# Kernel optimization log

Hardware: AMD Instinct MI355X
Metric: run time of the kernel (lower is better)

Reference implementation:

```python
import jax, jax.numpy as jnp
import numpy as np

V = 6890            # FAUST mesh vertices (also n_classes of the dense head)
C_IN = 3            # raw xyz signal
R, A = 5, 8         # kernel_size = (n_radial, n_angular)
ROT_DELTA = 1
ROTS = tuple(range(0, A, ROT_DELTA))  # 8 rotations
DIMS = [100, 100, 100]
EPS_BN = 1e-3       # keras BatchNormalization default epsilon


def setup_inputs() -> dict:
    key = jax.random.key(0)
    ks = jax.random.split(key, 12)
    inp = {}
    inp["signal"] = jax.random.normal(ks[0], (V, C_IN), jnp.float32)
    inp["bc_idx"] = jax.random.randint(ks[1], (V, R, A, 3), 0, V, dtype=jnp.int32)
    w = jax.random.uniform(ks[2], (V, R, A, 3), jnp.float32)
    inp["bc_w"] = w / jnp.sum(w, axis=-1, keepdims=True)  # convex barycentric weights
    # keras Normalization (not adapted): mean=0, var=1
    inp["norm_mean"] = jnp.zeros((C_IN,), jnp.float32)
    inp["norm_var"] = jnp.ones((C_IN,), jnp.float32)
    # ConvDirac templates: (amt_templates, n_radial, n_angular, c_in) + bias
    cins = [C_IN] + DIMS[:-1]
    for i, (ci, t) in enumerate(zip(cins, DIMS)):
        inp[f"w{i}"] = jax.random.normal(ks[3 + i], (t, R, A, ci), jnp.float32) * 0.05
        inp[f"b{i}"] = jnp.zeros((t,), jnp.float32)
    # BatchNorm (inference mode) params, stacked over the 3 blocks
    inp["bn_gamma"] = jnp.ones((3, DIMS[0]), jnp.float32)
    inp["bn_beta"] = jnp.zeros((3, DIMS[0]), jnp.float32)
    inp["bn_mean"] = jax.random.normal(ks[6], (3, DIMS[0]), jnp.float32) * 0.01
    inp["bn_var"] = jnp.ones((3, DIMS[0]), jnp.float32)
    inp["dense_w"] = jax.random.normal(ks[7], (DIMS[-1], V), jnp.float32) * 0.02
    inp["dense_b"] = jnp.zeros((V,), jnp.float32)
    return inp


def _isc_dirac(sig, bc_idx, bc_w, W, b):
    """Intrinsic surface conv (Dirac): barycentric patch gather + multi-rotation fold.
    sig: (V, C); bc_idx/bc_w: (V, R, A, 3); W: (T, R, A, C); b: (T,)
    returns (V, n_rot, T) after relu."""
    # patch operator: interpolate signal at template vertices -> (V, R, A, C)
    patch = jnp.einsum('vraic,vrai->vrac', sig[bc_idx], bc_w)
    # rotate the (small) template over the angular axis instead of the patch
    Wrot = jnp.stack([jnp.roll(W, -r, axis=2) for r in ROTS])  # (n_rot, T, R, A, C)
    out = jnp.einsum('vrac,ntrac->vnt', patch, Wrot) + b
    return jax.nn.relu(out)


def _amp(x):
    """AngularMaxPooling: keep the rotation response with max L2 norm. x: (V, n_rot, T)."""
    idx = jnp.argmax(jnp.linalg.norm(x, axis=-1), axis=-1)  # (V,)
    return jnp.take_along_axis(x, idx[:, None, None], axis=1)[:, 0, :]


def _bn(x, g, b, m, v):
    return g * (x - m) * jax.lax.rsqrt(v + EPS_BN) + b


def reference(signal, bc_idx, bc_w, norm_mean, norm_var, w0, b0, w1, b1, w2, b2,
              bn_gamma, bn_beta, bn_mean, bn_var, dense_w, dense_b):
    x = (signal - norm_mean) / jnp.sqrt(norm_var)
    for i, (W, b) in enumerate(((w0, b0), (w1, b1), (w2, b2))):
        x = _isc_dirac(x, bc_idx, bc_w, W, b)      # (V, n_rot, T)
        x = _amp(x)                                 # (V, T)
        x = _bn(x, bn_gamma[i], bn_beta[i], bn_mean[i], bn_var[i])
        # dropout: identity at inference
    return x @ dense_w + dense_b                    # (V, 6890)
```

## Files before the change

kernel.cpp:

```cpp
#include <hip/hip_runtime.h>

#define VN 6890
#define TN 100
#define NOUT 800
#define MP 6912
#define NP 896
#define CONVSZ (MP * NP)

typedef __attribute__((ext_vector_type(8))) short bf16x8;
typedef __attribute__((ext_vector_type(4))) float f32x4;

__device__ __forceinline__ unsigned short f2bf(float f) {
    unsigned u = __float_as_uint(f);
    return (unsigned short)((u + 0x7FFFu + ((u >> 16) & 1u)) >> 16);
}
__device__ __forceinline__ void split_bf16(float f, short* h, short* l) {
    unsigned short hb = f2bf(f);
    float hf = __uint_as_float(((unsigned)hb) << 16);
    *h = (short)hb;
    *l = (short)f2bf(f - hf);
}
__device__ __forceinline__ void gload16(const short* g, void* lds) {
    __builtin_amdgcn_global_load_lds(
        (const __attribute__((address_space(1))) void*)g,
        (__attribute__((address_space(3))) void*)lds, 16, 0, 0);
}

__global__ __launch_bounds__(256) void norm_kernel(
    const float* __restrict__ sig, const float* __restrict__ mean,
    const float* __restrict__ var, float* __restrict__ x0)
{
    int i = blockIdx.x * blockDim.x + threadIdx.x;
    if (i < VN * 3) {
        int c = i % 3;
        x0[i] = (sig[i] - mean[c]) / sqrtf(var[c]);
    }
}

template<int CIN, int KPAD>
__global__ __launch_bounds__(256) void rotw_split(
    const float* __restrict__ W, short* __restrict__ Bh, short* __restrict__ Bl)
{
    const int n = blockIdx.x;
    const int K = 40 * CIN;
    const int rot = n / TN, t = n - rot * TN;
    for (int k = threadIdx.x; k < KPAD; k += 256) {
        float w = 0.f;
        if (n < NOUT && k < K) {
            int ra = k / CIN, c = k - ra * CIN;
            int r = ra >> 3, a = ra & 7;
            int a2 = (a + rot) & 7;
            w = W[((t * 5 + r) * 8 + a2) * CIN + c];
        }
        short h, l; split_bf16(w, &h, &l);
        Bh[(size_t)n * KPAD + k] = h;
        Bl[(size_t)n * KPAD + k] = l;
    }
}

template<int CIN, int KPAD>
__global__ __launch_bounds__(256) void patch_split(
    const float* __restrict__ x, const int* __restrict__ bidx,
    const float* __restrict__ bw, short* __restrict__ Ph, short* __restrict__ Pl)
{
    __shared__ int   sIdx[120];
    __shared__ float sW[120];
    const int v = blockIdx.x;
    const int tid = threadIdx.x;
    const int K = 40 * CIN;
    if (v >= VN) {
        for (int e = tid; e < KPAD; e += 256) {
            Ph[(size_t)v * KPAD + e] = 0;
            Pl[(size_t)v * KPAD + e] = 0;
        }
        return;
    }
    if (tid < 120) { sIdx[tid] = bidx[v * 120 + tid]; sW[tid] = bw[v * 120 + tid]; }
    __syncthreads();
    for (int e = tid; e < KPAD; e += 256) {
        float s = 0.f;
        if (e < K) {
            int ra = e / CIN, c = e - ra * CIN;
            s = sW[ra * 3 + 0] * x[sIdx[ra * 3 + 0] * CIN + c]
              + sW[ra * 3 + 1] * x[sIdx[ra * 3 + 1] * CIN + c]
              + sW[ra * 3 + 2] * x[sIdx[ra * 3 + 2] * CIN + c];
        }
        short h, l; split_bf16(s, &h, &l);
        Ph[(size_t)v * KPAD + e] = h;
        Pl[(size_t)v * KPAD + e] = l;
    }
}

template<bool CONV_EPI>
__global__ __launch_bounds__(256, 2) void mfma_gemm(
    const short* __restrict__ Ah, const short* __restrict__ Al,
    const short* __restrict__ Bh, const short* __restrict__ Bl,
    const float* __restrict__ bias, float* __restrict__ C,
    int M, int N, int ldc, int K, int Ksl, int cstride)
{
    __shared__ __align__(16) short AhS[4096];
    __shared__ __align__(16) short AlS[4096];
    __shared__ __align__(16) short BhS[4096];
    __shared__ __align__(16) short BlS[4096];

    const int tid  = threadIdx.x;
    const int wave = tid >> 6;
    const int lane = tid & 63;
    const int lr = lane & 15, lg = lane >> 4;
    const int wm = wave >> 1, wn = wave & 1;
    const int m0 = blockIdx.x * 128;
    const int n0 = blockIdx.y * 128;
    const int kbase = blockIdx.z * Ksl;
    const int kcnt  = min(Ksl, K - kbase);
    if (CONV_EPI) C += (size_t)blockIdx.z * cstride;

    const int off0 = tid * 16, off1 = off0 + 4096;
    const int row0 = off0 >> 6, row1 = off1 >> 6;
    const int g0 = ((off0 >> 4) & 3) ^ ((row0 >> 1) & 3);
    const int g1 = ((off1 >> 4) & 3) ^ ((row1 >> 1) & 3);
    const size_t aO0 = (size_t)(m0 + row0) * K + kbase + g0 * 8;
    const size_t aO1 = (size_t)(m0 + row1) * K + kbase + g1 * 8;
    const size_t bO0 = (size_t)(n0 + row0) * K + kbase + g0 * 8;
    const size_t bO1 = (size_t)(n0 + row1) * K + kbase + g1 * 8;
    const int wofs = wave << 10;

    int aRd[4], bRd[4];
    #pragma unroll
    for (int f = 0; f < 4; ++f) {
        int ar = wm * 64 + f * 16 + lr;
        aRd[f] = ar * 64 + ((lg ^ ((ar >> 1) & 3)) << 4);
        int br = wn * 64 + f * 16 + lr;
        bRd[f] = br * 64 + ((lg ^ ((br >> 1) & 3)) << 4);
    }

    f32x4 acc[4][4];
    #pragma unroll
    for (int i = 0; i < 4; ++i)
        #pragma unroll
        for (int j = 0; j < 4; ++j)
            acc[i][j] = (f32x4){0.f, 0.f, 0.f, 0.f};

    const int nkt = kcnt >> 5;
    for (int kt = 0; kt < nkt; ++kt) {
        const int k0 = kt << 5;
        gload16(Ah + aO0 + k0, (char*)AhS + wofs);
        gload16(Ah + aO1 + k0, (char*)AhS + 4096 + wofs);
        gload16(Al + aO0 + k0, (char*)AlS + wofs);
        gload16(Al + aO1 + k0, (char*)AlS + 4096 + wofs);
        gload16(Bh + bO0 + k0, (char*)BhS + wofs);
        gload16(Bh + bO1 + k0, (char*)BhS + 4096 + wofs);
        gload16(Bl + bO0 + k0, (char*)BlS + wofs);
        gload16(Bl + bO1 + k0, (char*)BlS + 4096 + wofs);
        __syncthreads();

        bf16x8 ah[4], al[4], bh[4], bl[4];
        #pragma unroll
        for (int f = 0; f < 4; ++f) {
            ah[f] = *(const bf16x8*)((const char*)AhS + aRd[f]);
            al[f] = *(const bf16x8*)((const char*)AlS + aRd[f]);
            bh[f] = *(const bf16x8*)((const char*)BhS + bRd[f]);
            bl[f] = *(const bf16x8*)((const char*)BlS + bRd[f]);
        }
        #pragma unroll
        for (int i = 0; i < 4; ++i)
            #pragma unroll
            for (int j = 0; j < 4; ++j)
                acc[i][j] = __builtin_amdgcn_mfma_f32_16x16x32_bf16(ah[i], bh[j], acc[i][j], 0, 0, 0);
        #pragma unroll
        for (int i = 0; i < 4; ++i)
            #pragma unroll
            for (int j = 0; j < 4; ++j)
                acc[i][j] = __builtin_amdgcn_mfma_f32_16x16x32_bf16(ah[i], bl[j], acc[i][j], 0, 0, 0);
        #pragma unroll
        for (int i = 0; i < 4; ++i)
            #pragma unroll
            for (int j = 0; j < 4; ++j)
                acc[i][j] = __builtin_amdgcn_mfma_f32_16x16x32_bf16(al[i], bh[j], acc[i][j], 0, 0, 0);
        __syncthreads();
    }

    #pragma unroll
    for (int i = 0; i < 4; ++i) {
        const int mb = m0 + wm * 64 + i * 16 + lg * 4;
        #pragma unroll
        for (int j = 0; j < 4; ++j) {
            const int n = n0 + wn * 64 + j * 16 + lr;
            if (CONV_EPI) {
                #pragma unroll
                for (int q = 0; q < 4; ++q)
                    C[(size_t)(mb + q) * ldc + n] = acc[i][j][q];
            } else {
                if (n < N) {
                    const float bv = bias[n];
                    #pragma unroll
                    for (int q = 0; q < 4; ++q)
                        if (mb + q < M)
                            C[(size_t)(mb + q) * ldc + n] = acc[i][j][q] + bv;
                }
            }
        }
    }
}

template<bool CONV_EPI>
__global__ __launch_bounds__(256, 4) void tile_gemm(
    const float* __restrict__ A, const float* __restrict__ B,
    const float* __restrict__ bias, float* __restrict__ C,
    int M, int N, int K)
{
    __shared__ __align__(16) float As[32][132];
    __shared__ __align__(16) float Bs[32][68];

    const int tid = threadIdx.x;
    const int m0 = blockIdx.x * 128;
    const int n0 = blockIdx.y * 64;
    const int ty = tid >> 4;
    const int tx = tid & 15;
    const int nkt = (K + 31) >> 5;

    float4 aR[4];
    float2 bR[4];

    auto load_tile = [&](int kt) {
        const int k0 = kt << 5;
        #pragma unroll
        for (int j = 0; j < 4; ++j) {
            int q = tid + 256 * j;
            int row = q >> 3, kq = (q & 7) << 2;
            int v = m0 + row, k = k0 + kq;
            if (v < M && k < K)
                aR[j] = *reinterpret_cast<const float4*>(A + (size_t)v * K + k);
            else
                aR[j] = make_float4(0.f, 0.f, 0.f, 0.f);
        }
        #pragma unroll
        for (int j = 0; j < 2; ++j) {
            int q = tid + 256 * j;
            int krow = q >> 4, nq = (q & 15) << 2;
            int k = k0 + krow, n = n0 + nq;
            bR[2 * j]     = (k < K && n + 1 < N)
                ? *reinterpret_cast<const float2*>(B + (size_t)k * N + n)     : make_float2(0.f, 0.f);
            bR[2 * j + 1] = (k < K && n + 3 < N)
                ? *reinterpret_cast<const float2*>(B + (size_t)k * N + n + 2) : make_float2(0.f, 0.f);
        }
    };
    auto stage = [&]() {
        #pragma unroll
        for (int j = 0; j < 4; ++j) {
            int q = tid + 256 * j;
            int row = q >> 3, kq = (q & 7) << 2;
            As[kq + 0][row] = aR[j].x; As[kq + 1][row] = aR[j].y;
            As[kq + 2][row] = aR[j].z; As[kq + 3][row] = aR[j].w;
        }
        #pragma unroll
        for (int j = 0; j < 2; ++j) {
            int q = tid + 256 * j;
            int krow = q >> 4, nq = (q & 15) << 2;
            *reinterpret_cast<float2*>(&Bs[krow][nq])     = bR[2 * j];
            *reinterpret_cast<float2*>(&Bs[krow][nq + 2]) = bR[2 * j + 1];
        }
    };

    float acc[8][4];
    #pragma unroll
    for (int i = 0; i < 8; ++i)
        #pragma unroll
        for (int j = 0; j < 4; ++j) acc[i][j] = 0.f;

    load_tile(0);
    stage();
    __syncthreads();

    for (int kt = 0; kt < nkt; ++kt) {
        if (kt + 1 < nkt) load_tile(kt + 1);
        #pragma unroll 16
        for (int k = 0; k < 32; ++k) {
            float4 a0 = *reinterpret_cast<const float4*>(&As[k][ty * 8]);
            float4 a1 = *reinterpret_cast<const float4*>(&As[k][ty * 8 + 4]);
            float4 b  = *reinterpret_cast<const float4*>(&Bs[k][tx * 4]);
            float av[8] = {a0.x, a0.y, a0.z, a0.w, a1.x, a1.y, a1.z, a1.w};
            float bv[4] = {b.x, b.y, b.z, b.w};
            #pragma unroll
            for (int i = 0; i < 8; ++i)
                #pragma unroll
                for (int j = 0; j < 4; ++j)
                    acc[i][j] = fmaf(av[i], bv[j], acc[i][j]);
        }
        __syncthreads();
        if (kt + 1 < nkt) { stage(); __syncthreads(); }
    }

    #pragma unroll
    for (int i = 0; i < 8; ++i) {
        int vr = m0 + ty * 8 + i;
        if (vr >= M) continue;
        int nb = n0 + tx * 4;
        size_t base = (size_t)vr * N + nb;
        if (nb + 1 < N) {
            float2 o = {acc[i][0] + bias[nb], acc[i][1] + bias[nb + 1]};
            *reinterpret_cast<float2*>(C + base) = o;
        }
        if (nb + 3 < N) {
            float2 o = {acc[i][2] + bias[nb + 2], acc[i][3] + bias[nb + 3]};
            *reinterpret_cast<float2*>(C + base + 2) = o;
        }
    }
}

__global__ __launch_bounds__(256) void amp_bn(
    const float* __restrict__ conv,
    const float* __restrict__ bias,
    const float* __restrict__ g,  const float* __restrict__ be,
    const float* __restrict__ mu, const float* __restrict__ var,
    float* __restrict__ xout)
{
    int v = blockIdx.x * 4 + (threadIdx.x >> 6);
    int lane = threadIdx.x & 63;
    if (v >= VN) return;
    const float* y0 = conv + (size_t)v * NP;
    const float* y1 = y0 + CONVSZ;

    const float bLo = bias[lane];
    const float bHi = (lane < 36) ? bias[64 + lane] : 0.f;

    float t1[8], t2[8], s[8];
    #pragma unroll
    for (int n = 0; n < 8; ++n) {
        float a = fmaxf(y0[n * TN + lane] + y1[n * TN + lane] + bLo, 0.f);
        float b = (lane < 36)
            ? fmaxf(y0[n * TN + 64 + lane] + y1[n * TN + 64 + lane] + bHi, 0.f) : 0.f;
        t1[n] = a; t2[n] = b;
        s[n] = a * a + b * b;
    }
    #pragma unroll
    for (int off = 32; off > 0; off >>= 1)
        #pragma unroll
        for (int n = 0; n < 8; ++n) s[n] += __shfl_xor(s[n], off);

    int best = 0; float bs = s[0];
    #pragma unroll
    for (int n = 1; n < 8; ++n) { if (s[n] > bs) { bs = s[n]; best = n; } }

    float a = t1[0], b = t2[0];
    #pragma unroll
    for (int n = 1; n < 8; ++n) { if (best == n) { a = t1[n]; b = t2[n]; } }

    {
        float inv = 1.0f / sqrtf(var[lane] + 1e-3f);
        xout[v * TN + lane] = g[lane] * (a - mu[lane]) * inv + be[lane];
    }
    if (lane < 36) {
        int t = 64 + lane;
        float inv = 1.0f / sqrtf(var[t] + 1e-3f);
        xout[v * TN + t] = g[t] * (b - mu[t]) * inv + be[t];
    }
}

__global__ __launch_bounds__(256) void dense_a_split(
    const float* __restrict__ xA, short* __restrict__ Ah, short* __restrict__ Al)
{
    int i = blockIdx.x * 256 + threadIdx.x;
    if (i >= MP * 128) return;
    int v = i >> 7, k = i & 127;
    float f = (v < VN && k < TN) ? xA[v * TN + k] : 0.f;
    short h, l; split_bf16(f, &h, &l);
    Ah[i] = h; Al[i] = l;
}
__global__ __launch_bounds__(256) void dense_b_split(
    const float* __restrict__ dw, short* __restrict__ Bh, short* __restrict__ Bl)
{
    int i = blockIdx.x * 256 + threadIdx.x;
    if (i >= MP * 128) return;
    int n = i >> 7, k = i & 127;
    float f = (n < VN && k < TN) ? dw[(size_t)k * VN + n] : 0.f;
    short h, l; split_bf16(f, &h, &l);
    Bh[i] = h; Bl[i] = l;
}

extern "C" void kernel_launch(void* const* d_in, const int* in_sizes, int n_in,
                              void* d_out, int out_size, void* d_ws, size_t ws_size,
                              hipStream_t stream) {
    const float* signal = (const float*)d_in[0];
    const int*   bcix   = (const int*)  d_in[1];
    const float* bcw    = (const float*)d_in[2];
    const float* nmean  = (const float*)d_in[3];
    const float* nvar   = (const float*)d_in[4];
    const float* w0     = (const float*)d_in[5];
    const float* b0     = (const float*)d_in[6];
    const float* w1     = (const float*)d_in[7];
    const float* b1     = (const float*)d_in[8];
    const float* w2     = (const float*)d_in[9];
    const float* b2     = (const float*)d_in[10];
    const float* bng    = (const float*)d_in[11];
    const float* bnb    = (const float*)d_in[12];
    const float* bnm    = (const float*)d_in[13];
    const float* bnv    = (const float*)d_in[14];
    const float* dw     = (const float*)d_in[15];
    const float* db     = (const float*)d_in[16];
    float* out = (float*)d_out;

    float* x0 = (float*)d_ws;
    float* xA = x0 + 20736;
    float* xB = xA + 689024;
    short* dAh = (short*)xB;
    short* dAl = dAh + (size_t)MP * 128;
    short* dBh = dAl + (size_t)MP * 128;
    short* dBl = dBh + (size_t)MP * 128;
    const size_t ws_need = (size_t)709760 * 4 + (size_t)4 * MP * 128 * 2;
    const bool dense_mfma = ws_size >= ws_need;

    short* Ph  = (short*)out;
    short* Pl  = Ph  + (size_t)MP * 4000;
    short* Bth = Pl  + (size_t)MP * 4000;
    short* Btl = Bth + (size_t)NP * 4000;
    float* conv = out + (size_t)MP * 4000 + (size_t)NP * 4000;

    dim3 cgrid(MP / 128, NP / 128, 2);
    dim3 mgrid(MP / 128, MP / 128, 1);
    dim3 dgrid((VN + 127) / 128, (VN + 63) / 64);
    int ampg = (VN + 3) / 4;

    norm_kernel<<<(VN * 3 + 255) / 256, 256, 0, stream>>>(signal, nmean, nvar, x0);

    rotw_split<3, 128><<<NP, 256, 0, stream>>>(w0, Bth, Btl);
    patch_split<3, 128><<<MP, 256, 0, stream>>>(x0, bcix, bcw, Ph, Pl);
    mfma_gemm<true><<<cgrid, 256, 0, stream>>>(Ph, Pl, Bth, Btl, b0, conv, VN, NOUT, NP, 128, 64, CONVSZ);
    amp_bn<<<ampg, 256, 0, stream>>>(conv, b0, bng, bnb, bnm, bnv, xA);

    rotw_split<100, 4000><<<NP, 256, 0, stream>>>(w1, Bth, Btl);
    patch_split<100, 4000><<<MP, 256, 0, stream>>>(xA, bcix, bcw, Ph, Pl);
    mfma_gemm<true><<<cgrid, 256, 0, stream>>>(Ph, Pl, Bth, Btl, b1, conv, VN, NOUT, NP, 4000, 2016, CONVSZ);
    amp_bn<<<ampg, 256, 0, stream>>>(conv, b1, bng + 100, bnb + 100, bnm + 100, bnv + 100, xB);

    rotw_split<100, 4000><<<NP, 256, 0, stream>>>(w2, Bth, Btl);
    patch_split<100, 4000><<<MP, 256, 0, stream>>>(xB, bcix, bcw, Ph, Pl);
    mfma_gemm<true><<<cgrid, 256, 0, stream>>>(Ph, Pl, Bth, Btl, b2, conv, VN, NOUT, NP, 4000, 2016, CONVSZ);
    amp_bn<<<ampg, 256, 0, stream>>>(conv, b2, bng + 200, bnb + 200, bnm + 200, bnv + 200, xA);

    if (dense_mfma) {
        dense_a_split<<<(MP * 128 + 255) / 256, 256, 0, stream>>>(xA, dAh, dAl);
        dense_b_split<<<(MP * 128 + 255) / 256, 256, 0, stream>>>(dw, dBh, dBl);
        mfma_gemm<false><<<mgrid, 256, 0, stream>>>(dAh, dAl, dBh, dBl, db, out, VN, VN, VN, 128, 128, 0);
    } else {
        tile_gemm<false><<<dgrid, 256, 0, stream>>>(xA, dw, db, out, VN, VN, TN);
    }
}
```

Before: 756.3 us.

## Add 512-thread triple-buffered split-bf16 MFMA GEMM for hidden conv layers

Adds a new conv GEMM kernel that runs 8 waves per 128x128 tile. It uses a three-stage LDS ring filled by direct global-to-LDS loads, staggers the hi/lo operand loads between the three MFMA phases, and raises wave priority around the MFMA bursts. Layers 1 and 2 switch to this kernel, with the same split-K of 2. The aim is to hide global-load latency behind MFMA work in the dominant K=4000 GEMMs. In exchange it uses 96KB of LDS per block, runs one block per CU, and adds more barriers per k-step.

```diff
diff --git a/kernel.cpp b/kernel.cpp
--- a/kernel.cpp
+++ b/kernel.cpp
@@ -9,6 +9,8 @@
 
 typedef __attribute__((ext_vector_type(8))) short bf16x8;
 typedef __attribute__((ext_vector_type(4))) float f32x4;
+
+#define BAR() do { asm volatile("" ::: "memory"); __builtin_amdgcn_s_barrier(); asm volatile("" ::: "memory"); } while (0)
 
 __device__ __forceinline__ unsigned short f2bf(float f) {
     unsigned u = __float_as_uint(f);
@@ -202,6 +204,189 @@
     }
 }
 
+__global__ __launch_bounds__(512, 1) void mfma_conv512(
+    const short* __restrict__ Ah, const short* __restrict__ Al,
+    const short* __restrict__ Bh, const short* __restrict__ Bl,
+    float* __restrict__ C, int K, int Ksl, int cstride)
+{
+    __shared__ __align__(16) short LDS[3 * 4 * 4096];
+
+    const int tid = threadIdx.x;
+    const int w = tid >> 6, lane = tid & 63;
+    const int lr = lane & 15, lg = lane >> 4;
+    const int wm = w >> 2, wn = w & 3;
+    const int m0 = blockIdx.x * 128;
+    const int n0 = blockIdx.y * 128;
+    const int kbase = blockIdx.z * Ksl;
+    const int kcnt = min(Ksl, K - kbase);
+    C += (size_t)blockIdx.z * cstride;
+
+    const int srow = tid >> 2;
+    const int sg   = (tid & 3) ^ ((srow >> 1) & 3);
+    const size_t aO = (size_t)(m0 + srow) * K + kbase + sg * 8;
+    const size_t bO = (size_t)(n0 + srow) * K + kbase + sg * 8;
+    const int wdst = w << 9;
+
+    int aRd[4], bRd[2];
+    #pragma unroll
+    for (int i = 0; i < 4; ++i) {
+        int ar = wm * 64 + i * 16 + lr;
+        aRd[i] = ar * 64 + ((lg ^ ((ar >> 1) & 3)) << 4);
+    }
+    #pragma unroll
+    for (int j = 0; j < 2; ++j) {
+        int br = wn * 32 + j * 16 + lr;
+        bRd[j] = br * 64 + ((lg ^ ((br >> 1) & 3)) << 4);
+    }
+
+    f32x4 acc[4][2];
+    #pragma unroll
+    for (int i = 0; i < 4; ++i)
+        #pragma unroll
+        for (int j = 0; j < 2; ++j)
+            acc[i][j] = (f32x4){0.f, 0.f, 0.f, 0.f};
+
+    const int nt = kcnt >> 5;
+
+    auto REG = [&](int b, int r) -> short* { return &LDS[(b * 4 + r) * 4096]; };
+
+    {
+        gload16(Ah + aO,      REG(0, 0) + wdst);
+        gload16(Al + aO,      REG(0, 1) + wdst);
+        gload16(Bh + bO,      REG(0, 2) + wdst);
+        gload16(Bl + bO,      REG(0, 3) + wdst);
+        if (nt > 1) {
+            gload16(Ah + aO + 32, REG(1, 0) + wdst);
+            gload16(Al + aO + 32, REG(1, 1) + wdst);
+            gload16(Bh + bO + 32, REG(1, 2) + wdst);
+            gload16(Bl + bO + 32, REG(1, 3) + wdst);
+        }
+    }
+
+    int cur = 0;
+    for (int t = 0; t < nt; ++t) {
+        const char* LAh = (const char*)REG(cur, 0);
+        const char* LAl = (const char*)REG(cur, 1);
+        const char* LBh = (const char*)REG(cur, 2);
+        const char* LBl = (const char*)REG(cur, 3);
+        const int nb = (t + 2) % 3;
+        const int kn = (t + 2) << 5;
+
+        if (t + 2 < nt) {
+            gload16(Ah + aO + kn, REG(nb, 0) + wdst);
+            gload16(Bh + bO + kn, REG(nb, 2) + wdst);
+            asm volatile("s_waitcnt vmcnt(6)" ::: "memory");
+        } else if (t + 1 < nt) {
+            asm volatile("s_waitcnt vmcnt(4)" ::: "memory");
+        } else {
+            asm volatile("s_waitcnt vmcnt(0)" ::: "memory");
+        }
+        BAR();
+        bf16x8 ah[4], bh[2], bl[2], al[4];
+        #pragma unroll
+        for (int i = 0; i < 4; ++i) ah[i] = *(const bf16x8*)(LAh + aRd[i]);
+        #pragma unroll
+        for (int j = 0; j < 2; ++j) bh[j] = *(const bf16x8*)(LBh + bRd[j]);
+        __builtin_amdgcn_s_setprio(1);
+        #pragma unroll
+        for (int i = 0; i < 4; ++i)
+            #pragma unroll
+            for (int j = 0; j < 2; ++j)
+                acc[i][j] = __builtin_amdgcn_mfma_f32_16x16x32_bf16(ah[i], bh[j], acc[i][j], 0, 0, 0);
+        __builtin_amdgcn_s_setprio(0);
+        BAR();
+
+        #pragma unroll
+        for (int j = 0; j < 2; ++j) bl[j] = *(const bf16x8*)(LBl + bRd[j]);
+        if (t + 2 < nt) gload16(Al + aO + kn, REG(nb, 1) + wdst);
+        BAR();
+        __builtin_amdgcn_s_setprio(1);
+        #pragma unroll
+        for (int i = 0; i < 4; ++i)
+            #pragma unroll
+            for (int j = 0; j < 2; ++j)
+                acc[i][j] = __builtin_amdgcn_mfma_f32_16x16x32_bf16(ah[i], bl[j], acc[i][j], 0, 0, 0);
+        __builtin_amdgcn_s_setprio(0);
+        BAR();
+
+        #pragma unroll
+        for (int i = 0; i < 4; ++i) al[i] = *(const bf16x8*)(LAl + aRd[i]);
+        if (t + 2 < nt) gload16(Bl + bO + kn, REG(nb, 3) + wdst);
+        BAR();
+        __builtin_amdgcn_s_setprio(1);
+        #pragma unroll
+        for (int i = 0; i < 4; ++i)
+            #pragma unroll
+            for (int j = 0; j < 2; ++j)
+                acc[i][j] = __builtin_amdgcn_mfma_f32_16x16x32_bf16(al[i], bh[j], acc[i][j], 0, 0, 0);
+        __builtin_amdgcn_s_setprio(0);
+        BAR();
+
+        cur = (cur + 1 == 3) ? 0 : cur + 1;
+    }
+
+    #pragma unroll
+    for (int i = 0; i < 4; ++i) {
+        const int mb = m0 + wm * 64 + i * 16 + lg * 4;
+        #pragma unroll
+        for (int j = 0; j < 2; ++j) {
+            const int n = n0 + wn * 32 + j * 16 + lr;
+            #pragma unroll
+            for (int q = 0; q < 4; ++q)
+                C[(size_t)(mb + q) * NP + n] = acc[i][j][q];
+        }
+    }
+}
+
+__global__ __launch_bounds__(256) void amp_bn(
+    const float* __restrict__ conv,
+    const float* __restrict__ bias,
+    const float* __restrict__ g,  const float* __restrict__ be,
+    const float* __restrict__ mu, const float* __restrict__ var,
+    float* __restrict__ xout)
+{
+    int v = blockIdx.x * 4 + (threadIdx.x >> 6);
+    int lane = threadIdx.x & 63;
+    if (v >= VN) return;
+    const float* y0 = conv + (size_t)v * NP;
+    const float* y1 = y0 + CONVSZ;
+
+    const float bLo = bias[lane];
+    const float bHi = (lane < 36) ? bias[64 + lane] : 0.f;
+
+    float t1[8], t2[8], s[8];
+    #pragma unroll
+    for (int n = 0; n < 8; ++n) {
+        float a = fmaxf(y0[n * TN + lane] + y1[n * TN + lane] + bLo, 0.f);
+        float b = (lane < 36)
+            ? fmaxf(y0[n * TN + 64 + lane] + y1[n * TN + 64 + lane] + bHi, 0.f) : 0.f;
+        t1[n] = a; t2[n] = b;
+        s[n] = a * a + b * b;
+    }
+    #pragma unroll
+    for (int off = 32; off > 0; off >>= 1)
+        #pragma unroll
+        for (int n = 0; n < 8; ++n) s[n] += __shfl_xor(s[n], off);
+
+    int best = 0; float bs = s[0];
+    #pragma unroll
+    for (int n = 1; n < 8; ++n) { if (s[n] > bs) { bs = s[n]; best = n; } }
+
+    float a = t1[0], b = t2[0];
+    #pragma unroll
+    for (int n = 1; n < 8; ++n) { if (best == n) { a = t1[n]; b = t2[n]; } }
+
+    {
+        float inv = 1.0f / sqrtf(var[lane] + 1e-3f);
+        xout[v * TN + lane] = g[lane] * (a - mu[lane]) * inv + be[lane];
+    }
+    if (lane < 36) {
+        int t = 64 + lane;
+        float inv = 1.0f / sqrtf(var[t] + 1e-3f);
+        xout[v * TN + t] = g[t] * (b - mu[t]) * inv + be[t];
+    }
+}
+
 template<bool CONV_EPI>
 __global__ __launch_bounds__(256, 4) void tile_gemm(
     const float* __restrict__ A, const float* __restrict__ B,
@@ -304,55 +489,6 @@
             float2 o = {acc[i][2] + bias[nb + 2], acc[i][3] + bias[nb + 3]};
             *reinterpret_cast<float2*>(C + base + 2) = o;
         }
-    }
-}
-
-__global__ __launch_bounds__(256) void amp_bn(
-    const float* __restrict__ conv,
-    const float* __restrict__ bias,
-    const float* __restrict__ g,  const float* __restrict__ be,
-    const float* __restrict__ mu, const float* __restrict__ var,
-    float* __restrict__ xout)
-{
-    int v = blockIdx.x * 4 + (threadIdx.x >> 6);
-    int lane = threadIdx.x & 63;
-    if (v >= VN) return;
-    const float* y0 = conv + (size_t)v * NP;
-    const float* y1 = y0 + CONVSZ;
-
-    const float bLo = bias[lane];
-    const float bHi = (lane < 36) ? bias[64 + lane] : 0.f;
-
-    float t1[8], t2[8], s[8];
-    #pragma unroll
-    for (int n = 0; n < 8; ++n) {
-        float a = fmaxf(y0[n * TN + lane] + y1[n * TN + lane] + bLo, 0.f);
-        float b = (lane < 36)
-            ? fmaxf(y0[n * TN + 64 + lane] + y1[n * TN + 64 + lane] + bHi, 0.f) : 0.f;
-        t1[n] = a; t2[n] = b;
-        s[n] = a * a + b * b;
-    }
-    #pragma unroll
-    for (int off = 32; off > 0; off >>= 1)
-        #pragma unroll
-        for (int n = 0; n < 8; ++n) s[n] += __shfl_xor(s[n], off);
-
-    int best = 0; float bs = s[0];
-    #pragma unroll
-    for (int n = 1; n < 8; ++n) { if (s[n] > bs) { bs = s[n]; best = n; } }
-
-    float a = t1[0], b = t2[0];
-    #pragma unroll
-    for (int n = 1; n < 8; ++n) { if (best == n) { a = t1[n]; b = t2[n]; } }
-
-    {
-        float inv = 1.0f / sqrtf(var[lane] + 1e-3f);
-        xout[v * TN + lane] = g[lane] * (a - mu[lane]) * inv + be[lane];
-    }
-    if (lane < 36) {
-        int t = 64 + lane;
-        float inv = 1.0f / sqrtf(var[t] + 1e-3f);
-        xout[v * TN + t] = g[t] * (b - mu[t]) * inv + be[t];
     }
 }
 
@@ -416,6 +552,7 @@
     float* conv = out + (size_t)MP * 4000 + (size_t)NP * 4000;
 
     dim3 cgrid(MP / 128, NP / 128, 2);
+    dim3 c8grid(MP / 128, NP / 128, 2);
     dim3 mgrid(MP / 128, MP / 128, 1);
     dim3 dgrid((VN + 127) / 128, (VN + 63) / 64);
     int ampg = (VN + 3) / 4;
@@ -429,12 +566,12 @@
 
     rotw_split<100, 4000><<<NP, 256, 0, stream>>>(w1, Bth, Btl);
     patch_split<100, 4000><<<MP, 256, 0, stream>>>(xA, bcix, bcw, Ph, Pl);
-    mfma_gemm<true><<<cgrid, 256, 0, stream>>>(Ph, Pl, Bth, Btl, b1, conv, VN, NOUT, NP, 4000, 2016, CONVSZ);
+    mfma_conv512<<<c8grid, 512, 0, stream>>>(Ph, Pl, Bth, Btl, conv, 4000, 2016, CONVSZ);
     amp_bn<<<ampg, 256, 0, stream>>>(conv, b1, bng + 100, bnb + 100, bnm + 100, bnv + 100, xB);
 
     rotw_split<100, 4000><<<NP, 256, 0, stream>>>(w2, Bth, Btl);
     patch_split<100, 4000><<<MP, 256, 0, stream>>>(xB, bcix, bcw, Ph, Pl);
-    mfma_gemm<true><<<cgrid, 256, 0, stream>>>(Ph, Pl, Bth, Btl, b2, conv, VN, NOUT, NP, 4000, 2016, CONVSZ);
+    mfma_conv512<<<c8grid, 512, 0, stream>>>(Ph, Pl, Bth, Btl, conv, 4000, 2016, CONVSZ);
     amp_bn<<<ampg, 256, 0, stream>>>(conv, b2, bng + 200, bnb + 200, bnm + 200, bnv + 200, xA);
 
     if (dense_mfma) {
```

After: 742.3 us. Within noise of the previous version (-1.9%).

## Add triple-buffered split-bf16 MFMA GEMM for the 100-channel conv layers

Applied to the files above, without the earlier changes.

Adds a new conv_tri kernel for layers 1 and 2. It uses a three-stage LDS ring filled by direct global-to-LDS loads, with explicit vmcnt waits and a single barrier per K step, so the next two tiles load while MFMAs run. The launch grid is transposed (N-tiles on x, M-tiles on y), which changes block scheduling and cache reuse of the patch matrix. The trade-off is 96KB of LDS per block, which limits occupancy to one block per CU, plus a reliance on hand-placed waitcnt correctness.

```diff
diff --git a/kernel.cpp b/kernel.cpp
--- a/kernel.cpp
+++ b/kernel.cpp
@@ -9,6 +9,8 @@
 
 typedef __attribute__((ext_vector_type(8))) short bf16x8;
 typedef __attribute__((ext_vector_type(4))) float f32x4;
+
+#define BAR() do { asm volatile("" ::: "memory"); __builtin_amdgcn_s_barrier(); asm volatile("" ::: "memory"); } while (0)
 
 __device__ __forceinline__ unsigned short f2bf(float f) {
     unsigned u = __float_as_uint(f);
@@ -202,6 +204,163 @@
     }
 }
 
+__global__ __launch_bounds__(256, 1) void conv_tri(
+    const short* __restrict__ Ah, const short* __restrict__ Al,
+    const short* __restrict__ Bh, const short* __restrict__ Bl,
+    float* __restrict__ C, int K, int Ksl, int cstride)
+{
+    __shared__ __align__(16) short LDS[3 * 4 * 4096];
+
+    const int tid  = threadIdx.x;
+    const int wave = tid >> 6;
+    const int lane = tid & 63;
+    const int lr = lane & 15, lg = lane >> 4;
+    const int wm = wave >> 1, wn = wave & 1;
+    const int n0 = blockIdx.x * 128;
+    const int m0 = blockIdx.y * 128;
+    const int kbase = blockIdx.z * Ksl;
+    const int kcnt  = min(Ksl, K - kbase);
+    C += (size_t)blockIdx.z * cstride;
+
+    const int off0 = tid * 16, off1 = off0 + 4096;
+    const int row0 = off0 >> 6, row1 = off1 >> 6;
+    const int g0 = ((off0 >> 4) & 3) ^ ((row0 >> 1) & 3);
+    const int g1 = ((off1 >> 4) & 3) ^ ((row1 >> 1) & 3);
+    const size_t aO0 = (size_t)(m0 + row0) * K + kbase + g0 * 8;
+    const size_t aO1 = (size_t)(m0 + row1) * K + kbase + g1 * 8;
+    const size_t bO0 = (size_t)(n0 + row0) * K + kbase + g0 * 8;
+    const size_t bO1 = (size_t)(n0 + row1) * K + kbase + g1 * 8;
+    const int wofs = wave << 10;
+
+    int aRd[4], bRd[4];
+    #pragma unroll
+    for (int f = 0; f < 4; ++f) {
+        int ar = wm * 64 + f * 16 + lr;
+        aRd[f] = ar * 64 + ((lg ^ ((ar >> 1) & 3)) << 4);
+        int br = wn * 64 + f * 16 + lr;
+        bRd[f] = br * 64 + ((lg ^ ((br >> 1) & 3)) << 4);
+    }
+
+    f32x4 acc[4][4];
+    #pragma unroll
+    for (int i = 0; i < 4; ++i)
+        #pragma unroll
+        for (int j = 0; j < 4; ++j)
+            acc[i][j] = (f32x4){0.f, 0.f, 0.f, 0.f};
+
+    const int nt = kcnt >> 5;
+
+    auto issue = [&](int x) {
+        char* buf = (char*)LDS + (x % 3) * 32768;
+        const int k0 = x << 5;
+        gload16(Ah + aO0 + k0, buf + wofs);
+        gload16(Ah + aO1 + k0, buf + 4096 + wofs);
+        gload16(Al + aO0 + k0, buf + 8192 + wofs);
+        gload16(Al + aO1 + k0, buf + 8192 + 4096 + wofs);
+        gload16(Bh + bO0 + k0, buf + 16384 + wofs);
+        gload16(Bh + bO1 + k0, buf + 16384 + 4096 + wofs);
+        gload16(Bl + bO0 + k0, buf + 24576 + wofs);
+        gload16(Bl + bO1 + k0, buf + 24576 + 4096 + wofs);
+    };
+
+    issue(0);
+    if (nt > 1) issue(1);
+
+    for (int t = 0; t < nt; ++t) {
+        if (t + 1 < nt) { asm volatile("s_waitcnt vmcnt(8)" ::: "memory"); }
+        else            { asm volatile("s_waitcnt vmcnt(0)" ::: "memory"); }
+        BAR();
+
+        const char* buf = (const char*)LDS + (t % 3) * 32768;
+        bf16x8 ah[4], al[4], bh[4], bl[4];
+        #pragma unroll
+        for (int f = 0; f < 4; ++f) {
+            ah[f] = *(const bf16x8*)(buf + aRd[f]);
+            al[f] = *(const bf16x8*)(buf + 8192 + aRd[f]);
+            bh[f] = *(const bf16x8*)(buf + 16384 + bRd[f]);
+            bl[f] = *(const bf16x8*)(buf + 24576 + bRd[f]);
+        }
+        if (t + 2 < nt) issue(t + 2);
+
+        #pragma unroll
+        for (int i = 0; i < 4; ++i)
+            #pragma unroll
+            for (int j = 0; j < 4; ++j)
+                acc[i][j] = __builtin_amdgcn_mfma_f32_16x16x32_bf16(ah[i], bh[j], acc[i][j], 0, 0, 0);
+        #pragma unroll
+        for (int i = 0; i < 4; ++i)
+            #pragma unroll
+            for (int j = 0; j < 4; ++j)
+                acc[i][j] = __builtin_amdgcn_mfma_f32_16x16x32_bf16(ah[i], bl[j], acc[i][j], 0, 0, 0);
+        #pragma unroll
+        for (int i = 0; i < 4; ++i)
+            #pragma unroll
+            for (int j = 0; j < 4; ++j)
+                acc[i][j] = __builtin_amdgcn_mfma_f32_16x16x32_bf16(al[i], bh[j], acc[i][j], 0, 0, 0);
+    }
+
+    #pragma unroll
+    for (int i = 0; i < 4; ++i) {
+        const int mb = m0 + wm * 64 + i * 16 + lg * 4;
+        #pragma unroll
+        for (int j = 0; j < 4; ++j) {
+            const int n = n0 + wn * 64 + j * 16 + lr;
+            #pragma unroll
+            for (int q = 0; q < 4; ++q)
+                C[(size_t)(mb + q) * NP + n] = acc[i][j][q];
+        }
+    }
+}
+
+__global__ __launch_bounds__(256) void amp_bn(
+    const float* __restrict__ conv,
+    const float* __restrict__ bias,
+    const float* __restrict__ g,  const float* __restrict__ be,
+    const float* __restrict__ mu, const float* __restrict__ var,
+    float* __restrict__ xout)
+{
+    int v = blockIdx.x * 4 + (threadIdx.x >> 6);
+    int lane = threadIdx.x & 63;
+    if (v >= VN) return;
+    const float* y0 = conv + (size_t)v * NP;
+    const float* y1 = y0 + CONVSZ;
+
+    const float bLo = bias[lane];
+    const float bHi = (lane < 36) ? bias[64 + lane] : 0.f;
+
+    float t1[8], t2[8], s[8];
+    #pragma unroll
+    for (int n = 0; n < 8; ++n) {
+        float a = fmaxf(y0[n * TN + lane] + y1[n * TN + lane] + bLo, 0.f);
+        float b = (lane < 36)
+            ? fmaxf(y0[n * TN + 64 + lane] + y1[n * TN + 64 + lane] + bHi, 0.f) : 0.f;
+        t1[n] = a; t2[n] = b;
+        s[n] = a * a + b * b;
+    }
+    #pragma unroll
+    for (int off = 32; off > 0; off >>= 1)
+        #pragma unroll
+        for (int n = 0; n < 8; ++n) s[n] += __shfl_xor(s[n], off);
+
+    int best = 0; float bs = s[0];
+    #pragma unroll
+    for (int n = 1; n < 8; ++n) { if (s[n] > bs) { bs = s[n]; best = n; } }
+
+    float a = t1[0], b = t2[0];
+    #pragma unroll
+    for (int n = 1; n < 8; ++n) { if (best == n) { a = t1[n]; b = t2[n]; } }
+
+    {
+        float inv = 1.0f / sqrtf(var[lane] + 1e-3f);
+        xout[v * TN + lane] = g[lane] * (a - mu[lane]) * inv + be[lane];
+    }
+    if (lane < 36) {
+        int t = 64 + lane;
+        float inv = 1.0f / sqrtf(var[t] + 1e-3f);
+        xout[v * TN + t] = g[t] * (b - mu[t]) * inv + be[t];
+    }
+}
+
 template<bool CONV_EPI>
 __global__ __launch_bounds__(256, 4) void tile_gemm(
     const float* __restrict__ A, const float* __restrict__ B,
@@ -304,55 +463,6 @@
             float2 o = {acc[i][2] + bias[nb + 2], acc[i][3] + bias[nb + 3]};
             *reinterpret_cast<float2*>(C + base + 2) = o;
         }
-    }
-}
-
-__global__ __launch_bounds__(256) void amp_bn(
-    const float* __restrict__ conv,
-    const float* __restrict__ bias,
-    const float* __restrict__ g,  const float* __restrict__ be,
-    const float* __restrict__ mu, const float* __restrict__ var,
-    float* __restrict__ xout)
-{
-    int v = blockIdx.x * 4 + (threadIdx.x >> 6);
-    int lane = threadIdx.x & 63;
-    if (v >= VN) return;
-    const float* y0 = conv + (size_t)v * NP;
-    const float* y1 = y0 + CONVSZ;
-
-    const float bLo = bias[lane];
-    const float bHi = (lane < 36) ? bias[64 + lane] : 0.f;
-
-    float t1[8], t2[8], s[8];
-    #pragma unroll
-    for (int n = 0; n < 8; ++n) {
-        float a = fmaxf(y0[n * TN + lane] + y1[n * TN + lane] + bLo, 0.f);
-        float b = (lane < 36)
-            ? fmaxf(y0[n * TN + 64 + lane] + y1[n * TN + 64 + lane] + bHi, 0.f) : 0.f;
-        t1[n] = a; t2[n] = b;
-        s[n] = a * a + b * b;
-    }
-    #pragma unroll
-    for (int off = 32; off > 0; off >>= 1)
-        #pragma unroll
-        for (int n = 0; n < 8; ++n) s[n] += __shfl_xor(s[n], off);
-
-    int best = 0; float bs = s[0];
-    #pragma unroll
-    for (int n = 1; n < 8; ++n) { if (s[n] > bs) { bs = s[n]; best = n; } }
-
-    float a = t1[0], b = t2[0];
-    #pragma unroll
-    for (int n = 1; n < 8; ++n) { if (best == n) { a = t1[n]; b = t2[n]; } }
-
-    {
-        float inv = 1.0f / sqrtf(var[lane] + 1e-3f);
-        xout[v * TN + lane] = g[lane] * (a - mu[lane]) * inv + be[lane];
-    }
-    if (lane < 36) {
-        int t = 64 + lane;
-        float inv = 1.0f / sqrtf(var[t] + 1e-3f);
-        xout[v * TN + t] = g[t] * (b - mu[t]) * inv + be[t];
     }
 }
 
@@ -416,6 +526,7 @@
     float* conv = out + (size_t)MP * 4000 + (size_t)NP * 4000;
 
     dim3 cgrid(MP / 128, NP / 128, 2);
+    dim3 tgrid(NP / 128, MP / 128, 2);
     dim3 mgrid(MP / 128, MP / 128, 1);
     dim3 dgrid((VN + 127) / 128, (VN + 63) / 64);
     int ampg = (VN + 3) / 4;
@@ -429,12 +540,12 @@
 
     rotw_split<100, 4000><<<NP, 256, 0, stream>>>(w1, Bth, Btl);
     patch_split<100, 4000><<<MP, 256, 0, stream>>>(xA, bcix, bcw, Ph, Pl);
-    mfma_gemm<true><<<cgrid, 256, 0, stream>>>(Ph, Pl, Bth, Btl, b1, conv, VN, NOUT, NP, 4000, 2016, CONVSZ);
+    conv_tri<<<tgrid, 256, 0, stream>>>(Ph, Pl, Bth, Btl, conv, 4000, 2016, CONVSZ);
     amp_bn<<<ampg, 256, 0, stream>>>(conv, b1, bng + 100, bnb + 100, bnm + 100, bnv + 100, xB);
 
     rotw_split<100, 4000><<<NP, 256, 0, stream>>>(w2, Bth, Btl);
     patch_split<100, 4000><<<MP, 256, 0, stream>>>(xB, bcix, bcw, Ph, Pl);
-    mfma_gemm<true><<<cgrid, 256, 0, stream>>>(Ph, Pl, Bth, Btl, b2, conv, VN, NOUT, NP, 4000, 2016, CONVSZ);
+    conv_tri<<<tgrid, 256, 0, stream>>>(Ph, Pl, Bth, Btl, conv, 4000, 2016, CONVSZ);
     amp_bn<<<ampg, 256, 0, stream>>>(conv, b2, bng + 200, bnb + 200, bnm + 200, bnv + 200, xA);
 
     if (dense_mfma) {
```

Result: faster. 740.9 us (-2.0%).
